# Kernel tuning notes

Hardware: AMD Instinct MI355X
Metric: run time of the kernel (lower is better)

The kernel has to match this reference:

```python
import jax, jax.numpy as jnp
import numpy as np

N = 20000      # nodes
E = 320000     # edges (avg degree 16)
F_IN = 14
F_OUT = 9
H = 128        # hidden
L = 6          # message passing layers
ED = 3         # edge_dim
MSG_IN = 2 * H + ED  # 259


def _w(k, shape):
    return jax.random.normal(k, shape, jnp.float32) / np.sqrt(shape[0]).astype(np.float32)


def setup_inputs() -> dict:
    key = jax.random.key(0)
    ks = jax.random.split(key, 16)
    x = jax.random.normal(ks[0], (N, F_IN), jnp.float32)
    edge_index = jax.random.randint(ks[1], (2, E), 0, N, jnp.int64)
    edge_attr = jax.random.normal(ks[2], (E, ED), jnp.float32)
    # encoder: Linear(14,128) -> SiLU -> Linear(128,128)
    enc_w1 = _w(ks[3], (F_IN, H)); enc_b1 = jnp.zeros((H,), jnp.float32)
    enc_w2 = _w(ks[4], (H, H));    enc_b2 = jnp.zeros((H,), jnp.float32)
    # L EdgeConv layers: MLP(259->128) -> SiLU -> (128->128), stacked on leading dim
    kc = jax.random.split(ks[5], 2 * L)
    conv_w1 = jnp.stack([_w(kc[i], (MSG_IN, H)) for i in range(L)])
    conv_b1 = jnp.zeros((L, H), jnp.float32)
    conv_w2 = jnp.stack([_w(kc[L + i], (H, H)) for i in range(L)])
    conv_b2 = jnp.zeros((L, H), jnp.float32)
    # decoder: 128->128 SiLU 128->64 SiLU 64->9
    dec_w1 = _w(ks[6], (H, H));       dec_b1 = jnp.zeros((H,), jnp.float32)
    dec_w2 = _w(ks[7], (H, H // 2));  dec_b2 = jnp.zeros((H // 2,), jnp.float32)
    dec_w3 = _w(ks[8], (H // 2, F_OUT)); dec_b3 = jnp.zeros((F_OUT,), jnp.float32)
    return dict(x=x, edge_index=edge_index, edge_attr=edge_attr,
                enc_w1=enc_w1, enc_b1=enc_b1, enc_w2=enc_w2, enc_b2=enc_b2,
                conv_w1=conv_w1, conv_b1=conv_b1, conv_w2=conv_w2, conv_b2=conv_b2,
                dec_w1=dec_w1, dec_b1=dec_b1, dec_w2=dec_w2, dec_b2=dec_b2,
                dec_w3=dec_w3, dec_b3=dec_b3)


def _mlp2(x, w1, b1, w2, b2):
    return jnp.dot(jax.nn.silu(jnp.dot(x, w1) + b1), w2) + b2


def reference(x, edge_index, edge_attr,
              enc_w1, enc_b1, enc_w2, enc_b2,
              conv_w1, conv_b1, conv_w2, conv_b2,
              dec_w1, dec_b1, dec_w2, dec_b2, dec_w3, dec_b3):
    src, dst = edge_index[0], edge_index[1]
    # in-degree for mean aggregation (computed once; structure is fixed)
    deg = jnp.maximum(
        jax.ops.segment_sum(jnp.ones((E,), jnp.float32), dst, num_segments=N), 1.0)
    h = _mlp2(x, enc_w1, enc_b1, enc_w2, enc_b2)  # (N, H)
    for l in range(L):
        # gather-compute-scatter EdgeConv: msg MLP on [h_dst, h_src, edge_attr]
        m_in = jnp.concatenate([h[dst], h[src], edge_attr], axis=-1)  # (E, 2H+ED)
        m = _mlp2(m_in, conv_w1[l], conv_b1[l], conv_w2[l], conv_b2[l])  # (E, H)
        agg = jax.ops.segment_sum(m, dst, num_segments=N) / deg[:, None]  # (N, H)
        h = h + agg  # residual; dropout is identity in eval mode
    h = jax.nn.silu(jnp.dot(h, dec_w1) + dec_b1)
    h = jax.nn.silu(jnp.dot(h, dec_w2) + dec_b2)
    return jnp.dot(h, dec_w3) + dec_b3  # (N, F_OUT)
```

## Files before the change

### kernel.cpp

```cpp
#include <hip/hip_runtime.h>
#include <hip/hip_bf16.h>

#define NN 20000
#define EE 320000
#define HD 128

typedef _Float16 half8 __attribute__((ext_vector_type(8)));
typedef _Float16 half4 __attribute__((ext_vector_type(4)));
typedef _Float16 half2v __attribute__((ext_vector_type(2)));
typedef float floatx4 __attribute__((ext_vector_type(4)));
typedef float float2v __attribute__((ext_vector_type(2)));

__device__ __forceinline__ float silu_f(float x){
  float e = __expf(-x);
  return x * __builtin_amdgcn_rcpf(1.f + e);
}

__device__ __forceinline__ bool ei_is64(const int* __restrict__ ei){
  return (ei[1] | ei[3] | ei[5] | ei[7]) == 0;
}
__device__ __forceinline__ int ei_src(const int* __restrict__ ei, int e, bool is64){
  return is64 ? ei[2*(size_t)e] : ei[e];
}
__device__ __forceinline__ int ei_dst(const int* __restrict__ ei, int e, bool is64){
  return is64 ? ei[2*(size_t)EE + 2*(size_t)e] : ei[EE + e];
}

__global__ __launch_bounds__(256) void sentinel_kernel(float* __restrict__ out, int n, float val){
  int i = blockIdx.x*256 + threadIdx.x;
  if (i < n) out[i] = val;
}

__global__ __launch_bounds__(256) void pack_all_kernel(const float* __restrict__ cw1,
                                                       const float* __restrict__ cw2,
                                                       const float* __restrict__ dw1,
                                                       const float* __restrict__ dw2,
                                                       _Float16* __restrict__ w1p,
                                                       _Float16* __restrict__ w2p,
                                                       _Float16* __restrict__ w1dp,
                                                       _Float16* __restrict__ w2dp,
                                                       int* __restrict__ cur){
  int idx = blockIdx.x*256 + threadIdx.x;
  if (idx >= 319488){
    int j = idx - 319488;
    if (j < NN) cur[j] = 0;
    return;
  }
  if (idx < 196608){
    int j   = idx & 7;
    int ln  = (idx >> 3) & 63;
    int rest= idx >> 9;
    int cb  = rest & 15;
    int rest2 = rest >> 4;
    int ks  = rest2 & 3;
    int l   = rest2 >> 2;
    int k = ks*32 + (ln>>4)*8 + j;
    int c = cb*16 + (ln&15);
    float v = (c < 128) ? cw1[(size_t)l*33152 + (size_t)k*128 + c]
                        : cw1[(size_t)l*33152 + (size_t)(128+k)*128 + (c-128)];
    w1p[idx] = (_Float16)v;
  } else if (idx < 294912){
    int t = idx - 196608;
    int j   = t & 7;
    int ln  = (t >> 3) & 63;
    int rest= t >> 9;
    int cb  = rest & 7;
    int rest2 = rest >> 3;
    int ks  = rest2 & 3;
    int l   = rest2 >> 2;
    int k = ks*32 + (ln>>4)*8 + j;
    int c = cb*16 + (ln&15);
    w2p[t] = (_Float16)cw2[(size_t)l*16384 + (size_t)k*128 + c];
  } else {
    int t2 = idx - 294912;
    if (t2 < 16384){
      int j = t2 & 7, ln = (t2>>3)&63, cb = (t2>>9)&7, ks = t2>>12;
      int k = ks*32 + (ln>>4)*8 + j;
      int c = cb*16 + (ln&15);
      w1dp[t2] = (_Float16)dw1[(size_t)k*128 + c];
    } else {
      int t = t2 - 16384;
      int j = t & 7, ln = (t>>3)&63, cb = (t>>9)&3, ks = t>>11;
      int k = ks*32 + (ln>>4)*8 + j;
      int c = cb*16 + (ln&15);
      w2dp[t] = (_Float16)dw2[(size_t)k*64 + c];
    }
  }
}

__global__ __launch_bounds__(256) void count_kernel(const int* __restrict__ ei, int* __restrict__ cnt){
  int e = blockIdx.x*256 + threadIdx.x;
  bool is64 = ei_is64(ei);
  atomicAdd(&cnt[ei_dst(ei, e, is64)], 1);
}

__global__ __launch_bounds__(1024) void scan_kernel(int* __restrict__ cntcur,
                                                    int* __restrict__ row_start,
                                                    float* __restrict__ invd){
  __shared__ int part[1024];
  const int t = threadIdx.x;
  const int base = t*20;
  int loc[20];
  int sum = 0;
  #pragma unroll
  for (int i=0;i<20;++i){
    int n = base+i;
    int v = (n < NN) ? cntcur[n] : 0;
    loc[i] = sum; sum += v;
  }
  part[t] = sum;
  __syncthreads();
  for (int off=1; off<1024; off<<=1){
    int v = (t >= off) ? part[t-off] : 0;
    __syncthreads();
    part[t] += v;
    __syncthreads();
  }
  int pre = (t > 0) ? part[t-1] : 0;
  #pragma unroll
  for (int i=0;i<20;++i){
    int n = base+i;
    if (n < NN){
      int rs = pre + loc[i];
      int deg = ((i<19)?loc[i+1]:sum) - loc[i];
      row_start[n] = rs;
      invd[n] = (deg > 0) ? 1.f/(float)deg : 0.f;
      cntcur[n] = rs;
    }
  }
  if (t == 1023) row_start[NN] = part[1023];
}

__global__ __launch_bounds__(256) void scatter_kernel(const int* __restrict__ ei,
                                                      const float* __restrict__ eattr,
                                                      int* __restrict__ cur,
                                                      int4* __restrict__ rec){
  int e = blockIdx.x*256 + threadIdx.x;
  bool is64 = ei_is64(ei);
  int s = ei_src(ei, e, is64);
  int d = ei_dst(ei, e, is64);
  int pos = atomicAdd(&cur[d], 1);
  int4 r;
  r.x = __float_as_int(eattr[(size_t)e*3+0]);
  r.y = __float_as_int(eattr[(size_t)e*3+1]);
  r.z = __float_as_int(eattr[(size_t)e*3+2]);
  r.w = s*256;
  rec[pos] = r;
}

__global__ __launch_bounds__(128) void encoder_kernel(
    const float* __restrict__ x, const float* __restrict__ w1, const float* __restrict__ b1,
    const float* __restrict__ w2, const float* __restrict__ b2,
    float* __restrict__ h, _Float16* __restrict__ hh)
{
  __shared__ float xs[16][14];
  __shared__ float s1[16][128];
  const int n0 = blockIdx.x*16;
  const int tid = threadIdx.x;
  for (int idx=tid; idx<224; idx+=128){
    int i = idx/14, k = idx%14;
    xs[i][k] = x[(size_t)(n0+i)*14 + k];
  }
  __syncthreads();
  const int o = tid;
  float acc[16];
  float bv = b1[o];
  #pragma unroll
  for (int i=0;i<16;++i) acc[i] = bv;
  for (int k=0;k<14;++k){
    float w = w1[k*128+o];
    #pragma unroll
    for (int i=0;i<16;++i) acc[i] += xs[i][k]*w;
  }
  #pragma unroll
  for (int i=0;i<16;++i) s1[i][o] = silu_f(acc[i]);
  __syncthreads();
  float bv2 = b2[o];
  #pragma unroll
  for (int i=0;i<16;++i) acc[i] = bv2;
  for (int k=0;k<128;k+=4){
    float w0=w2[(k+0)*128+o], w1v=w2[(k+1)*128+o], w2v=w2[(k+2)*128+o], w3v=w2[(k+3)*128+o];
    #pragma unroll
    for (int i=0;i<16;++i){
      float4 sv = *(const float4*)&s1[i][k];
      acc[i] += sv.x*w0 + sv.y*w1v + sv.z*w2v + sv.w*w3v;
    }
  }
  #pragma unroll
  for (int i=0;i<16;++i){
    size_t off = (size_t)(n0+i)*HD + o;
    h[off] = acc[i];
    hh[off] = (_Float16)acc[i];
  }
}

__global__ __launch_bounds__(256) void proj_kernel(
    const _Float16* __restrict__ hh, const _Float16* __restrict__ w1p,
    const float* __restrict__ b1, _Float16* __restrict__ UV)
{
  const int tid = threadIdx.x;
  const int wv  = tid >> 6;
  const int ln  = tid & 63;
  const int q   = ln >> 4;
  const int m   = ln & 15;
  const int n0  = blockIdx.x*16;

  floatx4 acc[4];
  #pragma unroll
  for (int j=0;j<4;++j) acc[j] = (floatx4){0.f,0.f,0.f,0.f};

  #pragma unroll
  for (int ks=0; ks<4; ++ks){
    half8 a = *(const half8*)(hh + (size_t)(n0+m)*HD + ks*32 + q*8);
    const _Float16* wb = w1p + (size_t)(ks*16*64 + ln)*8;
    #pragma unroll
    for (int j=0; j<4; ++j){
      half8 b = *(const half8*)(wb + (size_t)(wv*4+j)*512);
      acc[j] = __builtin_amdgcn_mfma_f32_16x16x32_f16(a, b, acc[j], 0,0,0);
    }
  }
  #pragma unroll
  for (int j=0; j<4; ++j){
    const int c = (wv*4+j)*16 + m;
    const float bias = (c < 128) ? b1[c] : 0.f;
    #pragma unroll
    for (int r=0;r<4;++r)
      UV[(size_t)(n0+q*4+r)*256 + c] = (_Float16)(acc[j][r] + bias);
  }
}

__device__ __forceinline__ float2v edge_contrib(int4 r, half2v v, float2v u,
                                                float2v wc0, float2v wc1, float2v wc2){
  float2v p = u;
  p += __int_as_float(r.x) * wc0;
  p += __int_as_float(r.y) * wc1;
  p += __int_as_float(r.z) * wc2;
  p[0] += (float)v[0];
  p[1] += (float)v[1];
  float2v s;
  s[0] = silu_f(p[0]);
  s[1] = silu_f(p[1]);
  return s;
}

__global__ __launch_bounds__(256) void edge_agg_kernel(
    const _Float16* __restrict__ UV, const int* __restrict__ row_start,
    const int4* __restrict__ rec,
    const float* __restrict__ w1e, const float* __restrict__ invd,
    _Float16* __restrict__ S)
{
  const int tid = threadIdx.x;
  const int wv  = __builtin_amdgcn_readfirstlane(tid >> 6);
  const int ln  = tid & 63;
  const int n   = blockIdx.x*4 + wv;
  const int c0  = ln*2;

  const float2v wc0 = *(const float2v*)(w1e +   0 + c0);
  const float2v wc1 = *(const float2v*)(w1e + 128 + c0);
  const float2v wc2 = *(const float2v*)(w1e + 256 + c0);

  half2v uvp = *(const half2v*)(UV + (size_t)n*256 + c0);
  float2v u; u[0] = (float)uvp[0]; u[1] = (float)uvp[1];

  const int rs = row_start[n], re = row_start[n+1];
  float2v a0 = {0.f,0.f}, a1 = {0.f,0.f}, a2 = {0.f,0.f}, a3 = {0.f,0.f};

  const int nq = (re - rs) >> 2;
  int e = rs;
  for (int q = 0; q < nq; ++q, e += 4){
    const int4 r0 = rec[e+0];
    const int4 r1 = rec[e+1];
    const int4 r2 = rec[e+2];
    const int4 r3 = rec[e+3];
    const half2v v0 = *(const half2v*)(UV + (size_t)r0.w + 128 + c0);
    const half2v v1 = *(const half2v*)(UV + (size_t)r1.w + 128 + c0);
    const half2v v2 = *(const half2v*)(UV + (size_t)r2.w + 128 + c0);
    const half2v v3 = *(const half2v*)(UV + (size_t)r3.w + 128 + c0);
    a0 += edge_contrib(r0, v0, u, wc0, wc1, wc2);
    a1 += edge_contrib(r1, v1, u, wc0, wc1, wc2);
    a2 += edge_contrib(r2, v2, u, wc0, wc1, wc2);
    a3 += edge_contrib(r3, v3, u, wc0, wc1, wc2);
  }
  if (e < re){
    const int e1 = (e+1 < re) ? e+1 : e;
    const int e2 = (e+2 < re) ? e+2 : e;
    const int4 r0 = rec[e];
    const int4 r1 = rec[e1];
    const int4 r2 = rec[e2];
    const half2v v0 = *(const half2v*)(UV + (size_t)r0.w + 128 + c0);
    const half2v v1 = *(const half2v*)(UV + (size_t)r1.w + 128 + c0);
    const half2v v2 = *(const half2v*)(UV + (size_t)r2.w + 128 + c0);
    a0 += edge_contrib(r0, v0, u, wc0, wc1, wc2);
    if (e+1 < re) a1 += edge_contrib(r1, v1, u, wc0, wc1, wc2);
    if (e+2 < re) a2 += edge_contrib(r2, v2, u, wc0, wc1, wc2);
  }
  float2v a = (a0 + a1) + (a2 + a3);
  const float iv = invd[n];
  half2v outv; outv[0] = (_Float16)(a[0]*iv); outv[1] = (_Float16)(a[1]*iv);
  *(half2v*)(S + (size_t)n*HD + c0) = outv;
}

__global__ __launch_bounds__(256) void node_proj_kernel(
    const _Float16* __restrict__ S, const _Float16* __restrict__ w2p,
    const float* __restrict__ b2, const float* __restrict__ invd,
    float* __restrict__ h, _Float16* __restrict__ hh,
    const _Float16* __restrict__ w1pn, const float* __restrict__ b1n,
    _Float16* __restrict__ UV, int do_proj,
    const _Float16* __restrict__ w1dp, const float* __restrict__ db1,
    const _Float16* __restrict__ w2dp, const float* __restrict__ db2,
    const float* __restrict__ dw3, const float* __restrict__ db3,
    float* __restrict__ out, int do_dec)
{
  __shared__ _Float16 hl[16][136];
  __shared__ _Float16 d1[16][136];
  __shared__ float s2m[16][66];
  const int tid = threadIdx.x;
  const int wv  = tid >> 6;
  const int ln  = tid & 63;
  const int q   = ln >> 4;
  const int m   = ln & 15;
  const int n0  = blockIdx.x*16;

  floatx4 acc[2];
  acc[0] = (floatx4){0.f,0.f,0.f,0.f};
  acc[1] = (floatx4){0.f,0.f,0.f,0.f};
  #pragma unroll
  for (int ks=0; ks<4; ++ks){
    half8 a = *(const half8*)(S + (size_t)(n0+m)*HD + ks*32 + q*8);
    const _Float16* wb = w2p + (size_t)(ks*8*64 + ln)*8;
    #pragma unroll
    for (int j=0;j<2;++j){
      half8 b = *(const half8*)(wb + (size_t)(wv*2+j)*512);
      acc[j] = __builtin_amdgcn_mfma_f32_16x16x32_f16(a, b, acc[j], 0,0,0);
    }
  }
  float gate[4];
  #pragma unroll
  for (int r=0;r<4;++r) gate[r] = (invd[n0 + q*4 + r] > 0.f) ? 1.f : 0.f;
  #pragma unroll
  for (int j=0; j<2; ++j){
    const int c = (wv*2+j)*16 + m;
    const float bv = b2[c];
    #pragma unroll
    for (int r=0;r<4;++r){
      size_t off = (size_t)(n0+q*4+r)*HD + c;
      float hv = h[off] + acc[j][r] + gate[r]*bv;
      h[off] = hv;
      hh[off] = (_Float16)hv;
      hl[q*4+r][c] = (_Float16)hv;
    }
  }
  __syncthreads();

  if (do_proj){
    floatx4 acc2[4];
    #pragma unroll
    for (int j=0;j<4;++j) acc2[j] = (floatx4){0.f,0.f,0.f,0.f};
    #pragma unroll
    for (int ks=0; ks<4; ++ks){
      half8 a = *(const half8*)&hl[m][ks*32 + q*8];
      const _Float16* wb = w1pn + (size_t)(ks*16*64 + ln)*8;
      #pragma unroll
      for (int j=0; j<4; ++j){
        half8 b = *(const half8*)(wb + (size_t)(wv*4+j)*512);
        acc2[j] = __builtin_amdgcn_mfma_f32_16x16x32_f16(a, b, acc2[j], 0,0,0);
      }
    }
    #pragma unroll
    for (int j=0; j<4; ++j){
      const int c = (wv*4+j)*16 + m;
      const float bias = (c < 128) ? b1n[c] : 0.f;
      #pragma unroll
      for (int r=0;r<4;++r)
        UV[(size_t)(n0+q*4+r)*256 + c] = (_Float16)(acc2[j][r] + bias);
    }
  }

  if (do_dec){
    floatx4 acc1[2];
    acc1[0] = (floatx4){0.f,0.f,0.f,0.f};
    acc1[1] = (floatx4){0.f,0.f,0.f,0.f};
    #pragma unroll
    for (int ks=0; ks<4; ++ks){
      half8 a = *(const half8*)&hl[m][ks*32 + q*8];
      const _Float16* wb = w1dp + (size_t)(ks*8*64 + ln)*8;
      #pragma unroll
      for (int j=0; j<2; ++j){
        half8 b = *(const half8*)(wb + (size_t)(wv*2+j)*512);
        acc1[j] = __builtin_amdgcn_mfma_f32_16x16x32_f16(a, b, acc1[j], 0,0,0);
      }
    }
    #pragma unroll
    for (int j=0; j<2; ++j){
      const int c = (wv*2+j)*16 + m;
      const float bv = db1[c];
      #pragma unroll
      for (int r=0;r<4;++r)
        d1[q*4+r][c] = (_Float16)silu_f(acc1[j][r] + bv);
    }
    __syncthreads();

    floatx4 acc2 = (floatx4){0.f,0.f,0.f,0.f};
    #pragma unroll
    for (int ks=0; ks<4; ++ks){
      half8 a = *(const half8*)&d1[m][ks*32 + q*8];
      const _Float16* wb = w2dp + (size_t)(ks*4*64 + ln)*8;
      half8 b = *(const half8*)(wb + (size_t)wv*512);
      acc2 = __builtin_amdgcn_mfma_f32_16x16x32_f16(a, b, acc2, 0,0,0);
    }
    {
      const int c = wv*16 + m;
      const float bv = db2[c];
      #pragma unroll
      for (int r=0;r<4;++r)
        s2m[q*4+r][c] = silu_f(acc2[r] + bv);
    }
    __syncthreads();

    if (tid < 144){
      int i = tid/9, oo = tid%9;
      float a = db3[oo];
      #pragma unroll 8
      for (int k=0;k<64;++k) a += s2m[i][k]*dw3[k*9+oo];
      out[(size_t)(n0+i)*9 + oo] = a;
    }
  }
}

constexpr size_t OFF_H    = 0;
constexpr size_t OFF_HH   = 10240000;
constexpr size_t OFF_UV   = 15360000;
constexpr size_t OFF_S    = 25600000;
constexpr size_t OFF_INVD = 30720000;
constexpr size_t OFF_RS   = 30800000;
constexpr size_t OFF_CUR  = 30880064;
constexpr size_t OFF_REC  = 30960064;
constexpr size_t OFF_W1P  = 36080064;
constexpr size_t OFF_W2P  = 36473280;
constexpr size_t OFF_DW1P = 36669888;
constexpr size_t OFF_DW2P = 36702656;
constexpr size_t WS_NEEDED= 36719040;

extern "C" void kernel_launch(void* const* d_in, const int* in_sizes, int n_in,
                              void* d_out, int out_size, void* d_ws, size_t ws_size,
                              hipStream_t stream)
{
  float* out = (float*)d_out;
  const int nout_blk = (out_size + 255)/256;

  static const int EXP_SIZES[17] = {280000,640000,960000,1792,128,16384,128,
                                    198912,768,98304,768,16384,128,8192,64,576,9};
  if (n_in != 17){
    sentinel_kernel<<<nout_blk, 256, 0, stream>>>(out, out_size, 2.0e7f + (float)n_in*1.0e3f);
    return;
  }
  for (int i = 0; i < 17; ++i){
    if (in_sizes[i] != EXP_SIZES[i]){
      int sz = in_sizes[i] < 99999 ? in_sizes[i] : 99999;
      sentinel_kernel<<<nout_blk, 256, 0, stream>>>(out, out_size,
          1.0e7f + (float)i*1.0e5f + (float)sz);
      return;
    }
  }
  if (ws_size < WS_NEEDED){
    sentinel_kernel<<<nout_blk, 256, 0, stream>>>(out, out_size, 1.0e6f);
    return;
  }

  const float* x       = (const float*)d_in[0];
  const int*   ei      = (const int*)  d_in[1];
  const float* eattr   = (const float*)d_in[2];
  const float* enc_w1  = (const float*)d_in[3];
  const float* enc_b1  = (const float*)d_in[4];
  const float* enc_w2  = (const float*)d_in[5];
  const float* enc_b2  = (const float*)d_in[6];
  const float* conv_w1 = (const float*)d_in[7];
  const float* conv_b1 = (const float*)d_in[8];
  const float* conv_w2 = (const float*)d_in[9];
  const float* conv_b2 = (const float*)d_in[10];
  const float* dec_w1  = (const float*)d_in[11];
  const float* dec_b1  = (const float*)d_in[12];
  const float* dec_w2  = (const float*)d_in[13];
  const float* dec_b2  = (const float*)d_in[14];
  const float* dec_w3  = (const float*)d_in[15];
  const float* dec_b3  = (const float*)d_in[16];

  char* ws = (char*)d_ws;
  float*    h     = (float*)   (ws + OFF_H);
  _Float16* hh    = (_Float16*)(ws + OFF_HH);
  _Float16* UV    = (_Float16*)(ws + OFF_UV);
  _Float16* S     = (_Float16*)(ws + OFF_S);
  float*    invd  = (float*)   (ws + OFF_INVD);
  int*      rstart= (int*)     (ws + OFF_RS);
  int*      cur   = (int*)     (ws + OFF_CUR);
  int4*     rec   = (int4*)    (ws + OFF_REC);
  _Float16* w1p   = (_Float16*)(ws + OFF_W1P);
  _Float16* w2p   = (_Float16*)(ws + OFF_W2P);
  _Float16* w1dp  = (_Float16*)(ws + OFF_DW1P);
  _Float16* w2dp  = (_Float16*)(ws + OFF_DW2P);

  pack_all_kernel<<<1327, 256, 0, stream>>>(conv_w1, conv_w2, dec_w1, dec_w2,
                                            w1p, w2p, w1dp, w2dp, cur);
  count_kernel<<<EE/256, 256, 0, stream>>>(ei, cur);
  scan_kernel<<<1, 1024, 0, stream>>>(cur, rstart, invd);
  scatter_kernel<<<EE/256, 256, 0, stream>>>(ei, eattr, cur, rec);
  encoder_kernel<<<NN/16, 128, 0, stream>>>(x, enc_w1, enc_b1, enc_w2, enc_b2, h, hh);
  proj_kernel<<<NN/16, 256, 0, stream>>>(hh, w1p, conv_b1, UV);
  for (int l=0; l<6; ++l){
    edge_agg_kernel<<<NN/4, 256, 0, stream>>>(UV, rstart, rec,
                                              conv_w1 + (size_t)l*33152 + 32768,
                                              invd, S);
    const int lp = (l < 5) ? l+1 : 0;
    node_proj_kernel<<<NN/16, 256, 0, stream>>>(S, w2p + (size_t)l*16384,
                                                conv_b2 + (size_t)l*128, invd, h, hh,
                                                w1p + (size_t)lp*32768,
                                                conv_b1 + (size_t)lp*128,
                                                UV, (l < 5) ? 1 : 0,
                                                w1dp, dec_b1, w2dp, dec_b2,
                                                dec_w3, dec_b3, out,
                                                (l == 5) ? 1 : 0);
  }
}
```

Before: 405.3 us.

## Merge scatter into encoder launch and vectorize node residual update via LDS staging

```diff
diff --git a/kernel.cpp b/kernel.cpp
--- a/kernel.cpp
+++ b/kernel.cpp
@@ -131,32 +131,33 @@
   if (t == 1023) row_start[NN] = part[1023];
 }
 
-__global__ __launch_bounds__(256) void scatter_kernel(const int* __restrict__ ei,
-                                                      const float* __restrict__ eattr,
-                                                      int* __restrict__ cur,
-                                                      int4* __restrict__ rec){
-  int e = blockIdx.x*256 + threadIdx.x;
-  bool is64 = ei_is64(ei);
-  int s = ei_src(ei, e, is64);
-  int d = ei_dst(ei, e, is64);
-  int pos = atomicAdd(&cur[d], 1);
-  int4 r;
-  r.x = __float_as_int(eattr[(size_t)e*3+0]);
-  r.y = __float_as_int(eattr[(size_t)e*3+1]);
-  r.z = __float_as_int(eattr[(size_t)e*3+2]);
-  r.w = s*256;
-  rec[pos] = r;
-}
-
-__global__ __launch_bounds__(128) void encoder_kernel(
+__global__ __launch_bounds__(128) void scatter_encoder_kernel(
+    const int* __restrict__ ei, const float* __restrict__ eattr,
+    int* __restrict__ cur, int4* __restrict__ rec,
     const float* __restrict__ x, const float* __restrict__ w1, const float* __restrict__ b1,
     const float* __restrict__ w2, const float* __restrict__ b2,
     float* __restrict__ h, _Float16* __restrict__ hh)
 {
   __shared__ float xs[16][14];
   __shared__ float s1[16][128];
-  const int n0 = blockIdx.x*16;
   const int tid = threadIdx.x;
+
+  if (blockIdx.x < 2500){
+    int e = blockIdx.x*128 + tid;
+    bool is64 = ei_is64(ei);
+    int s = ei_src(ei, e, is64);
+    int d = ei_dst(ei, e, is64);
+    int pos = atomicAdd(&cur[d], 1);
+    int4 r;
+    r.x = __float_as_int(eattr[(size_t)e*3+0]);
+    r.y = __float_as_int(eattr[(size_t)e*3+1]);
+    r.z = __float_as_int(eattr[(size_t)e*3+2]);
+    r.w = s*256;
+    rec[pos] = r;
+    return;
+  }
+
+  const int n0 = (blockIdx.x - 2500)*16;
   for (int idx=tid; idx<224; idx+=128){
     int i = idx/14, k = idx%14;
     xs[i][k] = x[(size_t)(n0+i)*14 + k];
@@ -303,7 +304,7 @@
 __global__ __launch_bounds__(256) void node_proj_kernel(
     const _Float16* __restrict__ S, const _Float16* __restrict__ w2p,
     const float* __restrict__ b2, const float* __restrict__ invd,
-    float* __restrict__ h, _Float16* __restrict__ hh,
+    float* __restrict__ h,
     const _Float16* __restrict__ w1pn, const float* __restrict__ b1n,
     _Float16* __restrict__ UV, int do_proj,
     const _Float16* __restrict__ w1dp, const float* __restrict__ db1,
@@ -312,8 +313,11 @@
     float* __restrict__ out, int do_dec)
 {
   __shared__ _Float16 hl[16][136];
-  __shared__ _Float16 d1[16][136];
-  __shared__ float s2m[16][66];
+  __shared__ __align__(16) char ubuf[8576];
+  float    (*dl)[132]  = (float(*)[132])ubuf;
+  _Float16 (*d1)[136]  = (_Float16(*)[136])ubuf;
+  float    (*s2m)[66]  = (float(*)[66])(ubuf + 4352);
+
   const int tid = threadIdx.x;
   const int wv  = tid >> 6;
   const int ln  = tid & 63;
@@ -334,21 +338,38 @@
       acc[j] = __builtin_amdgcn_mfma_f32_16x16x32_f16(a, b, acc[j], 0,0,0);
     }
   }
-  float gate[4];
-  #pragma unroll
-  for (int r=0;r<4;++r) gate[r] = (invd[n0 + q*4 + r] > 0.f) ? 1.f : 0.f;
   #pragma unroll
   for (int j=0; j<2; ++j){
     const int c = (wv*2+j)*16 + m;
-    const float bv = b2[c];
-    #pragma unroll
-    for (int r=0;r<4;++r){
-      size_t off = (size_t)(n0+q*4+r)*HD + c;
-      float hv = h[off] + acc[j][r] + gate[r]*bv;
-      h[off] = hv;
-      hh[off] = (_Float16)hv;
-      hl[q*4+r][c] = (_Float16)hv;
-    }
+    #pragma unroll
+    for (int r=0;r<4;++r) dl[q*4+r][c] = acc[j][r];
+  }
+  __syncthreads();
+
+  {
+    const int idx = tid*8;
+    const int row = idx >> 7;
+    const int col = idx & 127;
+    const float g = (invd[n0 + row] > 0.f) ? 1.f : 0.f;
+    float4 h0 = *(const float4*)&h[(size_t)(n0+row)*HD + col];
+    float4 h1 = *(const float4*)&h[(size_t)(n0+row)*HD + col + 4];
+    float4 b0 = *(const float4*)&b2[col];
+    float4 b1v = *(const float4*)&b2[col + 4];
+    float4 d0 = *(const float4*)&dl[row][col];
+    float4 d1v = *(const float4*)&dl[row][col + 4];
+    h0.x += d0.x + g*b0.x;  h0.y += d0.y + g*b0.y;
+    h0.z += d0.z + g*b0.z;  h0.w += d0.w + g*b0.w;
+    h1.x += d1v.x + g*b1v.x; h1.y += d1v.y + g*b1v.y;
+    h1.z += d1v.z + g*b1v.z; h1.w += d1v.w + g*b1v.w;
+    if (!do_dec){
+      *(float4*)&h[(size_t)(n0+row)*HD + col]     = h0;
+      *(float4*)&h[(size_t)(n0+row)*HD + col + 4] = h1;
+    }
+    half4 p0, p1;
+    p0[0]=(_Float16)h0.x; p0[1]=(_Float16)h0.y; p0[2]=(_Float16)h0.z; p0[3]=(_Float16)h0.w;
+    p1[0]=(_Float16)h1.x; p1[1]=(_Float16)h1.y; p1[2]=(_Float16)h1.z; p1[3]=(_Float16)h1.w;
+    *(half4*)&hl[row][col]     = p0;
+    *(half4*)&hl[row][col + 4] = p1;
   }
   __syncthreads();
 
@@ -390,6 +411,7 @@
         acc1[j] = __builtin_amdgcn_mfma_f32_16x16x32_f16(a, b, acc1[j], 0,0,0);
       }
     }
+    __syncthreads();
     #pragma unroll
     for (int j=0; j<2; ++j){
       const int c = (wv*2+j)*16 + m;
@@ -503,8 +525,9 @@
                                             w1p, w2p, w1dp, w2dp, cur);
   count_kernel<<<EE/256, 256, 0, stream>>>(ei, cur);
   scan_kernel<<<1, 1024, 0, stream>>>(cur, rstart, invd);
-  scatter_kernel<<<EE/256, 256, 0, stream>>>(ei, eattr, cur, rec);
-  encoder_kernel<<<NN/16, 128, 0, stream>>>(x, enc_w1, enc_b1, enc_w2, enc_b2, h, hh);
+  scatter_encoder_kernel<<<3750, 128, 0, stream>>>(ei, eattr, cur, rec,
+                                                   x, enc_w1, enc_b1, enc_w2, enc_b2,
+                                                   h, hh);
   proj_kernel<<<NN/16, 256, 0, stream>>>(hh, w1p, conv_b1, UV);
   for (int l=0; l<6; ++l){
     edge_agg_kernel<<<NN/4, 256, 0, stream>>>(UV, rstart, rec,
@@ -512,7 +535,7 @@
                                               invd, S);
     const int lp = (l < 5) ? l+1 : 0;
     node_proj_kernel<<<NN/16, 256, 0, stream>>>(S, w2p + (size_t)l*16384,
-                                                conv_b2 + (size_t)l*128, invd, h, hh,
+                                                conv_b2 + (size_t)l*128, invd, h,
                                                 w1p + (size_t)lp*32768,
                                                 conv_b1 + (size_t)lp*128,
                                                 UV, (l < 5) ? 1 : 0,
```

After: 389.6 us. -3.9%, faster.
